# Performance work log

Hardware: AMD Instinct MI355X
Metric: run time of the kernel (lower is better)

Reference implementation:

```python
import jax, jax.numpy as jnp
import numpy as np

B, S, D, H, L = 2, 4096, 768, 12, 4
DFF, WIN, MAXPOS = 3072, 256, 4098
DH = D // H
W1 = WIN // 2            # one-sided window = 128
NC = S // W1             # number of query chunks = 32
EPS = 1e-12              # LongformerConfig default layer_norm_eps
SCALE = 1.0 / float(np.sqrt(DH))


def _ln(x, g, b):
    m = x.mean(-1, keepdims=True)
    v = ((x - m) ** 2).mean(-1, keepdims=True)
    return (x - m) / jnp.sqrt(v + EPS) * g + b


def _fwd(inputs, lengths, pos_emb, tok_emb, ln_emb_g, ln_emb_b,
         Wq, bq, Wk, bk, Wv, bv, Wo, bo, ln1_g, ln1_b,
         Wi, bi, Wf, bf, ln2_g, ln2_b):
    # embeddings: roberta-style position ids start at padding_idx+1 = 2
    x = inputs + pos_emb[2:2 + S][None] + tok_emb[0][None, None]
    x = _ln(x, ln_emb_g, ln_emb_b)

    mask = jnp.arange(S)[None, :] < lengths[:, None]            # [B,S] valid tokens
    idx = jnp.arange(NC)[:, None] * W1 + jnp.arange(3 * W1)     # [NC,3W] into padded keys
    jglob = idx - W1                                            # global key positions
    key_valid = (jglob >= 0)[None] & (jglob[None] < lengths[:, None, None])  # [B,NC,3W]
    qpos = jnp.arange(W1)[:, None]
    kpos = jnp.arange(3 * W1)[None, :]
    band = (kpos >= qpos) & (kpos <= qpos + 2 * W1)             # [W,3W] sliding band
    valid = band[None, None, None] & key_valid[:, None, :, None, :]  # [B,1,NC,W,3W]
    qmask = mask.reshape(B, NC, W1).astype(inputs.dtype)

    for l in range(L):
        q = (x @ Wq[l] + bq[l]).reshape(B, S, H, DH) * SCALE
        k = (x @ Wk[l] + bk[l]).reshape(B, S, H, DH)
        v = (x @ Wv[l] + bv[l]).reshape(B, S, H, DH)
        kp = jnp.pad(k, ((0, 0), (W1, W1), (0, 0), (0, 0)))
        vp = jnp.pad(v, ((0, 0), (W1, W1), (0, 0), (0, 0)))
        kc = jnp.take(kp, idx, axis=1)                          # [B,NC,3W,H,DH]
        vc = jnp.take(vp, idx, axis=1)
        qc = q.reshape(B, NC, W1, H, DH)
        scores = jnp.einsum('bcqhd,bckhd->bhcqk', qc, kc)       # [B,H,NC,W,3W]
        scores = jnp.where(valid, scores, -1e9)
        probs = jax.nn.softmax(scores, axis=-1)
        probs = probs * qmask[:, None, :, :, None]              # zero padded query rows (HF behavior)
        ctx = jnp.einsum('bhcqk,bckhd->bcqhd', probs, vc).reshape(B, S, D)
        x = _ln(x + ctx @ Wo[l] + bo[l], ln1_g[l], ln1_b[l])
        h = jax.nn.gelu(x @ Wi[l] + bi[l], approximate=False)
        x = _ln(x + h @ Wf[l] + bf[l], ln2_g[l], ln2_b[l])
    return x


def setup_inputs() -> dict:
    ks = jax.random.split(jax.random.key(0), 16)
    s = jnp.float32(0.02)
    f = jax.random.normal
    return {
        'inputs': f(ks[0], (B, S, D), jnp.float32),
        'lengths': jax.random.randint(ks[1], (B,), S // 2, S + 1),
        'pos_emb': s * f(ks[2], (MAXPOS, D), jnp.float32),
        'tok_emb': s * f(ks[3], (1, D), jnp.float32),
        'ln_emb_g': jnp.ones((D,), jnp.float32), 'ln_emb_b': jnp.zeros((D,), jnp.float32),
        'Wq': s * f(ks[4], (L, D, D), jnp.float32), 'bq': jnp.zeros((L, D), jnp.float32),
        'Wk': s * f(ks[5], (L, D, D), jnp.float32), 'bk': jnp.zeros((L, D), jnp.float32),
        'Wv': s * f(ks[6], (L, D, D), jnp.float32), 'bv': jnp.zeros((L, D), jnp.float32),
        'Wo': s * f(ks[7], (L, D, D), jnp.float32), 'bo': jnp.zeros((L, D), jnp.float32),
        'ln1_g': jnp.ones((L, D), jnp.float32), 'ln1_b': jnp.zeros((L, D), jnp.float32),
        'Wi': s * f(ks[8], (L, D, DFF), jnp.float32), 'bi': jnp.zeros((L, DFF), jnp.float32),
        'Wf': s * f(ks[9], (L, DFF, D), jnp.float32), 'bf': jnp.zeros((L, D), jnp.float32),
        'ln2_g': jnp.ones((L, D), jnp.float32), 'ln2_b': jnp.zeros((L, D), jnp.float32),
    }


def reference(inputs, lengths, pos_emb, tok_emb, ln_emb_g, ln_emb_b,
              Wq, bq, Wk, bk, Wv, bv, Wo, bo, ln1_g, ln1_b,
              Wi, bi, Wf, bf, ln2_g, ln2_b):
    return _fwd(inputs, lengths, pos_emb, tok_emb, ln_emb_g, ln_emb_b,
                Wq, bq, Wk, bk, Wv, bv, Wo, bo, ln1_g, ln1_b,
                Wi, bi, Wf, bf, ln2_g, ln2_b)
```

## Files before the change

### kernel.cpp

```cpp
#include <hip/hip_runtime.h>
#include <cstdint>

#define S_LEN 4096
#define D_MODEL 768
#define NHEAD 12
#define DHE 64
#define DFF_ 3072
#define NL 4
#define W1_ 128
#define NC_ 32
#define QKVN 2304

typedef __attribute__((ext_vector_type(8))) short v8s;
typedef __attribute__((ext_vector_type(4))) short v4s;
typedef __attribute__((ext_vector_type(4))) float v4f;

__device__ __forceinline__ short f2bf(float f) {
  union { float f; unsigned u; } x; x.f = f;
  unsigned r = x.u + 0x7fffu + ((x.u >> 16) & 1u);
  return (short)(r >> 16);
}

__device__ __forceinline__ float b2f(short s) {
  union { unsigned u; float f; } x; x.u = ((unsigned)(unsigned short)s) << 16;
  return x.f;
}

__device__ __forceinline__ void load_lds16(const short* g, short* l) {
  __builtin_amdgcn_global_load_lds((const __attribute__((address_space(1))) void*)g,
                                   (__attribute__((address_space(3))) void*)l, 16, 0, 0);
}

template<int EPI>
__global__ __launch_bounds__(256, 2)
void gemm128(const short* __restrict__ A, const short* __restrict__ Bt,
             const float* __restrict__ bias, void* __restrict__ outp,
             int M, int N, int K)
{
  __shared__ short sA[2][128 * 64];
  __shared__ short sB[2][128 * 64];
  const int tid = threadIdx.x;
  const int lane = tid & 63, wid = tid >> 6;
  const int g = lane >> 4, l16 = lane & 15;
  const int wr = wid >> 1, wc = wid & 1;
  const int nt = K >> 6;

  const int gx = gridDim.x;
  const int nwg = gx * gridDim.y;
  const int p = blockIdx.y * gx + blockIdx.x;
  const int q8 = nwg >> 3;
  const int lb = (p & 7) * q8 + (p >> 3);
  const int bn_ = lb % gx, bm_ = lb / gx;

  const short* Ab = A + (size_t)(bm_ * 128) * K;
  const short* Bb = Bt + (size_t)(bn_ * 128) * K;

  auto stage = [&](int t, int bufi) {
#pragma unroll
    for (int i = 0; i < 4; ++i) {
      const int byte = i * 4096 + tid * 16;
      const int row = byte >> 7;
      const int lir = (byte & 127) ^ ((row & 7) << 4);
      const int wbase = (i * 4096 + wid * 1024) >> 1;
      load_lds16(Ab + (size_t)row * K + t * 64 + (lir >> 1), &sA[bufi][wbase]);
    }
#pragma unroll
    for (int i = 0; i < 4; ++i) {
      const int byte = i * 4096 + tid * 16;
      const int row = byte >> 7;
      const int lir = (byte & 127) ^ ((row & 7) << 4);
      const int wbase = (i * 4096 + wid * 1024) >> 1;
      load_lds16(Bb + (size_t)row * K + t * 64 + (lir >> 1), &sB[bufi][wbase]);
    }
  };

  auto ldf = [&](const short* plane, int row, int kk) -> v8s {
    const int b = (kk * 64 + g * 16) ^ ((row & 7) << 4);
    return *(const v8s*)((const char*)plane + row * 128 + b);
  };

  v4f acc[4][4] = {};

  stage(0, 0);
  stage(1, 1);
  asm volatile("s_waitcnt vmcnt(8)" ::: "memory");
  __builtin_amdgcn_s_barrier();

  for (int t = 0; t < nt; ++t) {
    const int cur = t & 1;
    const short* pA = sA[cur];
    const short* pB = sB[cur];
    v8s fa[2][4], fb[2][4];
#pragma unroll
    for (int kk = 0; kk < 2; ++kk) {
#pragma unroll
      for (int m = 0; m < 4; ++m) fa[kk][m] = ldf(pA, wr * 64 + m * 16 + l16, kk);
#pragma unroll
      for (int n = 0; n < 4; ++n) fb[kk][n] = ldf(pB, wc * 64 + n * 16 + l16, kk);
    }
    asm volatile("s_waitcnt lgkmcnt(0)" ::: "memory");
    __builtin_amdgcn_sched_barrier(0);
    __builtin_amdgcn_s_barrier();
    if (t + 2 < nt) stage(t + 2, cur);
    __builtin_amdgcn_sched_barrier(0);
    __builtin_amdgcn_s_setprio(1);
#pragma unroll
    for (int kk = 0; kk < 2; ++kk)
#pragma unroll
      for (int m = 0; m < 4; ++m)
#pragma unroll
        for (int n = 0; n < 4; ++n)
          acc[m][n] = __builtin_amdgcn_mfma_f32_16x16x32_bf16(fa[kk][m], fb[kk][n], acc[m][n], 0, 0, 0);
    __builtin_amdgcn_s_setprio(0);
    __builtin_amdgcn_sched_barrier(0);
    if (t + 2 < nt)      asm volatile("s_waitcnt vmcnt(8)" ::: "memory");
    else if (t + 1 < nt) asm volatile("s_waitcnt vmcnt(0)" ::: "memory");
    if (t + 1 < nt) __builtin_amdgcn_s_barrier();
  }

  const int row0 = bm_ * 128 + wr * 64;
  const int col0 = bn_ * 128 + wc * 64;
#pragma unroll
  for (int m = 0; m < 4; ++m)
#pragma unroll
    for (int n = 0; n < 4; ++n) {
      const int col = col0 + n * 16 + l16;
      const float bc = bias[col];
#pragma unroll
      for (int r = 0; r < 4; ++r) {
        const int row = row0 + m * 16 + g * 4 + r;
        const float v = acc[m][n][r] + bc;
        if (EPI == 0) {
          ((short*)outp)[(size_t)row * N + col] = f2bf(v);
        } else {
          const float e = __expf(1.5957691216057308f * (v + 0.044715f * v * v * v));
          ((short*)outp)[(size_t)row * N + col] = f2bf(v - v / (1.0f + e));
        }
      }
    }
}

__global__ __launch_bounds__(256)
void transpose_w(const float* __restrict__ in, short* __restrict__ out, int K, int N,
                 size_t in_ls, size_t out_ls, float scale)
{
  __shared__ float t[32][33];
  const int n0 = blockIdx.x * 32, k0 = blockIdx.y * 32;
  const float* src = in + (size_t)blockIdx.z * in_ls;
  short* dst = out + (size_t)blockIdx.z * out_ls;
  const int tx = threadIdx.x, ty = threadIdx.y;
#pragma unroll
  for (int i = 0; i < 4; ++i)
    t[ty + 8*i][tx] = src[(size_t)(k0 + ty + 8*i) * N + n0 + tx];
  __syncthreads();
#pragma unroll
  for (int i = 0; i < 4; ++i)
    dst[(size_t)(n0 + ty + 8*i) * K + k0 + tx] = f2bf(t[tx][ty + 8*i] * scale);
}

__global__ void prep_bias(const float* __restrict__ bq, const float* __restrict__ bk,
                          const float* __restrict__ bv, float* __restrict__ out)
{
  const int l = blockIdx.x, p = blockIdx.y, c = threadIdx.x;
  const float* s = p == 0 ? bq : (p == 1 ? bk : bv);
  out[(l * 3 + p) * 768 + c] = s[l * 768 + c] * (p == 0 ? 0.125f : 1.0f);
}

__global__ __launch_bounds__(512)
void vtrans(const short* __restrict__ qkv, short* __restrict__ vt)
{
  __shared__ short t[64][65];
  const int s0 = blockIdx.x * 64, h = blockIdx.y, b = blockIdx.z;
  const int tx = threadIdx.x, ty = threadIdx.y;
#pragma unroll
  for (int i = 0; i < 8; ++i)
    t[ty + 8*i][tx] = qkv[(size_t)(b * S_LEN + s0 + ty + 8*i) * QKVN + 1536 + h * DHE + tx];
  __syncthreads();
#pragma unroll
  for (int i = 0; i < 8; ++i)
    vt[((size_t)(b * NHEAD + h) * DHE + ty + 8*i) * S_LEN + s0 + tx] = t[tx][ty + 8*i];
}

template<int MODE>
__global__ __launch_bounds__(256)
void ln_kernel(const float* __restrict__ in0, const void* __restrict__ in1,
               const float* __restrict__ in2,
               const float* __restrict__ gamma, const float* __restrict__ beta,
               float* __restrict__ outf, short* __restrict__ outb)
{
  __shared__ float red[8];
  const int row = blockIdx.x;
  const int tid = threadIdx.x;
  const int wave = tid >> 6, lane = tid & 63;
  float v[3];
#pragma unroll
  for (int i = 0; i < 3; ++i) {
    const int c = tid + i * 256;
    const size_t idx = (size_t)row * D_MODEL + c;
    if (MODE == 0) {
      const int s = row & (S_LEN - 1);
      v[i] = in0[idx] + ((const float*)in1)[(size_t)(2 + s) * D_MODEL + c] + in2[c];
    } else {
      v[i] = in0[idx] + b2f(((const short*)in1)[idx]);
    }
  }
  float sum = v[0] + v[1] + v[2];
#pragma unroll
  for (int m = 1; m < 64; m <<= 1) sum += __shfl_xor(sum, m, 64);
  if (lane == 0) red[wave] = sum;
  __syncthreads();
  const float mean = (red[0] + red[1] + red[2] + red[3]) * (1.0f / 768.0f);
  float sq = 0.f;
#pragma unroll
  for (int i = 0; i < 3; ++i) { float d = v[i] - mean; sq += d * d; }
#pragma unroll
  for (int m = 1; m < 64; m <<= 1) sq += __shfl_xor(sq, m, 64);
  if (lane == 0) red[4 + wave] = sq;
  __syncthreads();
  const float var = (red[4] + red[5] + red[6] + red[7]) * (1.0f / 768.0f);
  const float rstd = 1.0f / sqrtf(var + 1e-12f);
#pragma unroll
  for (int i = 0; i < 3; ++i) {
    const int c = tid + i * 256;
    const size_t idx = (size_t)row * D_MODEL + c;
    const float o = (v[i] - mean) * rstd * gamma[c] + beta[c];
    outf[idx] = o;
    outb[idx] = f2bf(o);
  }
}

__global__ __launch_bounds__(256, 2)
void att_fused(const short* __restrict__ qkv, const short* __restrict__ vt,
               const int* __restrict__ lengths, short* __restrict__ ctx)
{
  __shared__ __align__(16) short KP[320 * 64];
  __shared__ __align__(16) short Vl[64 * 320];
  const int p = blockIdx.x;
  const int lb = (p & 7) * 192 + (p >> 3);
  const int hq = lb & 1, c = (lb >> 1) & 31, bh = lb >> 6;
  const int b = bh / 12, h = bh - b * 12;
  const int len = lengths[b];
  const int tid = threadIdx.x;
  const int wave = tid >> 6, lane = tid & 63;
  const int g = lane >> 4, l16 = lane & 15;
  const int j0h = c * W1_ + hq * 64 - W1_;

  {
    const int row0 = tid >> 3;
    const int o = (tid & 7) * 16;
    const char* kcol = (const char*)qkv + (size_t)b * S_LEN * 4608 + 1536 + h * 128;
#pragma unroll
    for (int i = 0; i < 10; ++i) {
      const int r_ = i * 32 + row0;
      const int op = o ^ ((r_ & 7) << 4);
      int jg = j0h + r_;
      jg = jg < 0 ? 0 : (jg > S_LEN - 1 ? S_LEN - 1 : jg);
      load_lds16((const short*)(kcol + (size_t)jg * 4608 + op),
                 (short*)((char*)KP + i * 4096 + wave * 1024));
    }
  }
  {
    const char* vrow = (const char*)vt + ((size_t)(b * NHEAD + h) * DHE) * (S_LEN * 2);
#pragma unroll
    for (int r = 0; r < 10; ++r) {
      const int off = r * 4096 + tid * 16;
      const int rw = (int)(((unsigned)off * 6554u) >> 22);
      const int o = off - rw * 640;
      int jb = j0h * 2 + (o ^ ((rw & 7) << 4));
      jb = jb < 0 ? 0 : (jb > S_LEN * 2 - 16 ? S_LEN * 2 - 16 : jb);
      load_lds16((const short*)(vrow + (size_t)rw * (S_LEN * 2) + jb),
                 (short*)((char*)Vl + r * 4096 + wave * 1024));
    }
  }
  const int qrow = c * W1_ + hq * 64 + wave * 16 + l16;
  const short* qp = qkv + (size_t)(b * S_LEN + qrow) * QKVN + h * DHE;
  const v8s a0 = *(const v8s*)(qp + g * 8);
  const v8s a1 = *(const v8s*)(qp + 32 + g * 8);

  asm volatile("s_waitcnt vmcnt(0)" ::: "memory");
  __builtin_amdgcn_sched_barrier(0);
  __builtin_amdgcn_s_barrier();

  v4f s[20];
  const int kswz = (l16 & 7) << 4;
#pragma unroll
  for (int nt = 0; nt < 20; ++nt) {
    const char* krow = (const char*)KP + (nt * 16 + l16) * 128;
    const v8s k0 = *(const v8s*)(krow + ((g * 16) ^ kswz));
    const v8s k1 = *(const v8s*)(krow + ((64 + g * 16) ^ kswz));
    v4f t = {0.f, 0.f, 0.f, 0.f};
    t = __builtin_amdgcn_mfma_f32_16x16x32_bf16(k0, a0, t, 0, 0, 0);
    t = __builtin_amdgcn_mfma_f32_16x16x32_bf16(k1, a1, t, 0, 0, 0);
    s[nt] = t;
  }

  const int qloc = wave * 16 + l16;
  float m = -3.0e38f;
#pragma unroll
  for (int nt = 0; nt < 20; ++nt)
#pragma unroll
    for (int r = 0; r < 4; ++r) {
      const int j = nt * 16 + g * 4 + r;
      const int jg = j0h + j;
      const bool ok = (j >= qloc) & (j <= qloc + 2 * W1_) & (jg >= 0) & (jg < len);
      const float v = ok ? s[nt][r] : -1e9f;
      s[nt][r] = v;
      m = fmaxf(m, v);
    }
  m = fmaxf(m, __shfl_xor(m, 16, 64));
  m = fmaxf(m, __shfl_xor(m, 32, 64));
  float su = 0.f;
#pragma unroll
  for (int nt = 0; nt < 20; ++nt)
#pragma unroll
    for (int r = 0; r < 4; ++r) {
      const float e = __expf(s[nt][r] - m);
      s[nt][r] = e;
      su += e;
    }
  su += __shfl_xor(su, 16, 64);
  su += __shfl_xor(su, 32, 64);
  const float f = (qrow < len) ? 1.0f / su : 0.0f;

  __builtin_amdgcn_s_barrier();
  const int pswz = (qloc & 7) << 4;
  char* prow = (char*)KP + qloc * 640;
#pragma unroll
  for (int nt = 0; nt < 20; ++nt) {
    v4s pk;
#pragma unroll
    for (int r = 0; r < 4; ++r) pk[r] = f2bf(s[nt][r] * f);
    *(v4s*)(prow + ((nt * 32 + g * 8) ^ pswz)) = pk;
  }
  asm volatile("s_waitcnt lgkmcnt(0)" ::: "memory");
  __builtin_amdgcn_sched_barrier(0);

  v4f acc[4] = {};
#pragma unroll
  for (int kc = 0; kc < 10; ++kc) {
    const v8s fa = *(const v8s*)(prow + ((kc * 64 + g * 16) ^ pswz));
#pragma unroll
    for (int dt = 0; dt < 4; ++dt) {
      const int vr = dt * 16 + l16;
      const v8s fb = *(const v8s*)((char*)Vl + vr * 640 + ((kc * 64 + g * 16) ^ ((vr & 7) << 4)));
      acc[dt] = __builtin_amdgcn_mfma_f32_16x16x32_bf16(fa, fb, acc[dt], 0, 0, 0);
    }
  }
  const int srow0 = c * W1_ + hq * 64 + wave * 16;
#pragma unroll
  for (int dt = 0; dt < 4; ++dt)
#pragma unroll
    for (int r = 0; r < 4; ++r)
      ctx[(size_t)(b * S_LEN + srow0 + g * 4 + r) * D_MODEL + h * DHE + dt * 16 + l16] = f2bf(acc[dt][r]);
}

extern "C" void kernel_launch(void* const* d_in, const int* in_sizes, int n_in,
                              void* d_out, int out_size, void* d_ws, size_t ws_size,
                              hipStream_t stream) {
  (void)in_sizes; (void)n_in; (void)out_size; (void)ws_size;
  const float* inputs  = (const float*)d_in[0];
  const int*   lengths = (const int*)d_in[1];
  const float* pos_emb = (const float*)d_in[2];
  const float* tok_emb = (const float*)d_in[3];
  const float* ln_emb_g = (const float*)d_in[4];
  const float* ln_emb_b = (const float*)d_in[5];
  const float* Wq = (const float*)d_in[6];
  const float* bq = (const float*)d_in[7];
  const float* Wk = (const float*)d_in[8];
  const float* bk = (const float*)d_in[9];
  const float* Wv = (const float*)d_in[10];
  const float* bv = (const float*)d_in[11];
  const float* Wo = (const float*)d_in[12];
  const float* bo = (const float*)d_in[13];
  const float* ln1_g = (const float*)d_in[14];
  const float* ln1_b = (const float*)d_in[15];
  const float* Wi = (const float*)d_in[16];
  const float* bi = (const float*)d_in[17];
  const float* Wf = (const float*)d_in[18];
  const float* bf2 = (const float*)d_in[19];
  const float* ln2_g = (const float*)d_in[20];
  const float* ln2_b = (const float*)d_in[21];

  const size_t MTOK = (size_t)2 * S_LEN;
  const size_t DD  = (size_t)D_MODEL * D_MODEL;
  const size_t DDF = (size_t)D_MODEL * DFF_;

  char* ws = (char*)d_ws;
  size_t off = 0;
  auto alloc = [&](size_t bytes) { void* p = ws + off; off += (bytes + 255) & ~(size_t)255; return p; };

  short* xb    = (short*)alloc(MTOK * D_MODEL * 2);
  short* qkv   = (short*)alloc(MTOK * QKVN * 2);
  short* vtb   = (short*)alloc(MTOK * D_MODEL * 2);
  short* yb    = (short*)alloc(MTOK * D_MODEL * 2);
  short* ctxb  = (short*)alloc(MTOK * D_MODEL * 2);
  short* hb    = (short*)alloc(MTOK * DFF_ * 2);
  short* wqkvt = (short*)alloc((size_t)NL * QKVN * D_MODEL * 2);
  short* wot   = (short*)alloc((size_t)NL * DD * 2);
  short* wit   = (short*)alloc((size_t)NL * DDF * 2);
  short* wft   = (short*)alloc((size_t)NL * DDF * 2);
  float* bqkv  = (float*)alloc((size_t)NL * QKVN * 4);
  float* x = (float*)d_out;

  const dim3 tb(32, 8);
  const size_t QL = (size_t)QKVN * D_MODEL;
  transpose_w<<<dim3(24, 24, NL), tb, 0, stream>>>(Wq, wqkvt,            D_MODEL, D_MODEL, DD, QL, 0.125f);
  transpose_w<<<dim3(24, 24, NL), tb, 0, stream>>>(Wk, wqkvt + 768*768,  D_MODEL, D_MODEL, DD, QL, 1.0f);
  transpose_w<<<dim3(24, 24, NL), tb, 0, stream>>>(Wv, wqkvt + 1536*768, D_MODEL, D_MODEL, DD, QL, 1.0f);
  transpose_w<<<dim3(24, 24, NL), tb, 0, stream>>>(Wo, wot, D_MODEL, D_MODEL, DD, DD, 1.0f);
  transpose_w<<<dim3(96, 24, NL), tb, 0, stream>>>(Wi, wit, D_MODEL, DFF_, DDF, DDF, 1.0f);
  transpose_w<<<dim3(24, 96, NL), tb, 0, stream>>>(Wf, wft, DFF_, D_MODEL, DDF, DDF, 1.0f);
  prep_bias<<<dim3(NL, 3), 768, 0, stream>>>(bq, bk, bv, bqkv);

  ln_kernel<0><<<MTOK, 256, 0, stream>>>(inputs, pos_emb, tok_emb, ln_emb_g, ln_emb_b, x, xb);

  for (int l = 0; l < NL; ++l) {
    gemm128<0><<<dim3(18, 64), 256, 0, stream>>>(xb, wqkvt + (size_t)l * QL, bqkv + (size_t)l * QKVN,
                                                 qkv, (int)MTOK, QKVN, D_MODEL);
    vtrans<<<dim3(64, NHEAD, 2), dim3(64, 8), 0, stream>>>(qkv, vtb);
    att_fused<<<dim3(1536), 256, 0, stream>>>(qkv, vtb, lengths, ctxb);
    gemm128<0><<<dim3(6, 64), 256, 0, stream>>>(ctxb, wot + (size_t)l * DD, bo + l * D_MODEL,
                                                yb, (int)MTOK, D_MODEL, D_MODEL);
    ln_kernel<1><<<MTOK, 256, 0, stream>>>(x, yb, nullptr, ln1_g + l * D_MODEL, ln1_b + l * D_MODEL, x, xb);
    gemm128<2><<<dim3(24, 64), 256, 0, stream>>>(xb, wit + (size_t)l * DDF, bi + l * DFF_,
                                                 hb, (int)MTOK, DFF_, D_MODEL);
    gemm128<0><<<dim3(6, 64), 256, 0, stream>>>(hb, wft + (size_t)l * DDF, bf2 + l * D_MODEL,
                                                yb, (int)MTOK, D_MODEL, DFF_);
    ln_kernel<1><<<MTOK, 256, 0, stream>>>(x, yb, nullptr, ln2_g + l * D_MODEL, ln2_b + l * D_MODEL, x, xb);
  }
}
```

Before: 895.5 us.

## Use 128x64 GEMM tiles for N=768 projections and reorder the MFMA/stage pipeline

Templates the GEMM on N tile width so the two N=768 GEMMs (output projection and FFN down) use 128x64 tiles. That doubles their grid from 384 to 768 workgroups, which fills the CUs better, and raises the occupancy hint to 3. The main loop is also reordered: MFMAs now issue right after the LDS fragment reads, without an explicit lgkmcnt wait, and the next stage's global-to-LDS loads are issued after the barrier that follows the compute. This trades more A-tile reloads and less overlap of the prefetch with the MFMAs for better load balance.

```diff
diff --git a/kernel.cpp b/kernel.cpp
--- a/kernel.cpp
+++ b/kernel.cpp
@@ -31,14 +31,17 @@
                                    (__attribute__((address_space(3))) void*)l, 16, 0, 0);
 }
 
-template<int EPI>
-__global__ __launch_bounds__(256, 2)
+template<int NB, int EPI>
+__global__ __launch_bounds__(256, NB == 64 ? 3 : 2)
 void gemm128(const short* __restrict__ A, const short* __restrict__ Bt,
              const float* __restrict__ bias, void* __restrict__ outp,
              int M, int N, int K)
 {
+  constexpr int NF = NB / 32;
+  constexpr int BI = NB / 32;
+  constexpr int SI = 4 + BI;
   __shared__ short sA[2][128 * 64];
-  __shared__ short sB[2][128 * 64];
+  __shared__ short sB[2][NB * 64];
   const int tid = threadIdx.x;
   const int lane = tid & 63, wid = tid >> 6;
   const int g = lane >> 4, l16 = lane & 15;
@@ -53,7 +56,7 @@
   const int bn_ = lb % gx, bm_ = lb / gx;
 
   const short* Ab = A + (size_t)(bm_ * 128) * K;
-  const short* Bb = Bt + (size_t)(bn_ * 128) * K;
+  const short* Bb = Bt + (size_t)(bn_ * NB) * K;
 
   auto stage = [&](int t, int bufi) {
 #pragma unroll
@@ -65,7 +68,7 @@
       load_lds16(Ab + (size_t)row * K + t * 64 + (lir >> 1), &sA[bufi][wbase]);
     }
 #pragma unroll
-    for (int i = 0; i < 4; ++i) {
+    for (int i = 0; i < BI; ++i) {
       const int byte = i * 4096 + tid * 16;
       const int row = byte >> 7;
       const int lir = (byte & 127) ^ ((row & 7) << 4);
@@ -79,51 +82,58 @@
     return *(const v8s*)((const char*)plane + row * 128 + b);
   };
 
-  v4f acc[4][4] = {};
+  v4f acc[4][NF] = {};
 
   stage(0, 0);
   stage(1, 1);
-  asm volatile("s_waitcnt vmcnt(8)" ::: "memory");
+  if constexpr (NB == 128) asm volatile("s_waitcnt vmcnt(8)" ::: "memory");
+  else                     asm volatile("s_waitcnt vmcnt(6)" ::: "memory");
   __builtin_amdgcn_s_barrier();
+  __builtin_amdgcn_sched_barrier(0);
 
   for (int t = 0; t < nt; ++t) {
     const int cur = t & 1;
     const short* pA = sA[cur];
     const short* pB = sB[cur];
-    v8s fa[2][4], fb[2][4];
+    v8s fa[2][4], fb[2][NF];
 #pragma unroll
     for (int kk = 0; kk < 2; ++kk) {
 #pragma unroll
       for (int m = 0; m < 4; ++m) fa[kk][m] = ldf(pA, wr * 64 + m * 16 + l16, kk);
 #pragma unroll
-      for (int n = 0; n < 4; ++n) fb[kk][n] = ldf(pB, wc * 64 + n * 16 + l16, kk);
-    }
-    asm volatile("s_waitcnt lgkmcnt(0)" ::: "memory");
+      for (int n = 0; n < NF; ++n) fb[kk][n] = ldf(pB, wc * (NF * 16) + n * 16 + l16, kk);
+    }
+    __builtin_amdgcn_s_setprio(1);
+#pragma unroll
+    for (int kk = 0; kk < 2; ++kk)
+#pragma unroll
+      for (int m = 0; m < 4; ++m)
+#pragma unroll
+        for (int n = 0; n < NF; ++n)
+          acc[m][n] = __builtin_amdgcn_mfma_f32_16x16x32_bf16(fa[kk][m], fb[kk][n], acc[m][n], 0, 0, 0);
+    __builtin_amdgcn_s_setprio(0);
+    __builtin_amdgcn_s_barrier();
     __builtin_amdgcn_sched_barrier(0);
-    __builtin_amdgcn_s_barrier();
     if (t + 2 < nt) stage(t + 2, cur);
     __builtin_amdgcn_sched_barrier(0);
-    __builtin_amdgcn_s_setprio(1);
-#pragma unroll
-    for (int kk = 0; kk < 2; ++kk)
-#pragma unroll
-      for (int m = 0; m < 4; ++m)
-#pragma unroll
-        for (int n = 0; n < 4; ++n)
-          acc[m][n] = __builtin_amdgcn_mfma_f32_16x16x32_bf16(fa[kk][m], fb[kk][n], acc[m][n], 0, 0, 0);
-    __builtin_amdgcn_s_setprio(0);
-    __builtin_amdgcn_sched_barrier(0);
-    if (t + 2 < nt)      asm volatile("s_waitcnt vmcnt(8)" ::: "memory");
-    else if (t + 1 < nt) asm volatile("s_waitcnt vmcnt(0)" ::: "memory");
-    if (t + 1 < nt) __builtin_amdgcn_s_barrier();
+    if (t + 2 < nt) {
+      if constexpr (NB == 128) asm volatile("s_waitcnt vmcnt(8)" ::: "memory");
+      else                     asm volatile("s_waitcnt vmcnt(6)" ::: "memory");
+    } else if (t + 1 < nt) {
+      asm volatile("s_waitcnt vmcnt(0)" ::: "memory");
+    }
+    if (t + 1 < nt) {
+      __builtin_amdgcn_s_barrier();
+      __builtin_amdgcn_sched_barrier(0);
+    }
   }
 
   const int row0 = bm_ * 128 + wr * 64;
-  const int col0 = bn_ * 128 + wc * 64;
+  const int col0 = bn_ * NB + wc * (NF * 16);
 #pragma unroll
   for (int m = 0; m < 4; ++m)
 #pragma unroll
-    for (int n = 0; n < 4; ++n) {
+    for (int n = 0; n < NF; ++n) {
       const int col = col0 + n * 16 + l16;
       const float bc = bias[col];
 #pragma unroll
@@ -415,17 +425,17 @@
   ln_kernel<0><<<MTOK, 256, 0, stream>>>(inputs, pos_emb, tok_emb, ln_emb_g, ln_emb_b, x, xb);
 
   for (int l = 0; l < NL; ++l) {
-    gemm128<0><<<dim3(18, 64), 256, 0, stream>>>(xb, wqkvt + (size_t)l * QL, bqkv + (size_t)l * QKVN,
-                                                 qkv, (int)MTOK, QKVN, D_MODEL);
+    gemm128<128, 0><<<dim3(18, 64), 256, 0, stream>>>(xb, wqkvt + (size_t)l * QL, bqkv + (size_t)l * QKVN,
+                                                      qkv, (int)MTOK, QKVN, D_MODEL);
     vtrans<<<dim3(64, NHEAD, 2), dim3(64, 8), 0, stream>>>(qkv, vtb);
     att_fused<<<dim3(1536), 256, 0, stream>>>(qkv, vtb, lengths, ctxb);
-    gemm128<0><<<dim3(6, 64), 256, 0, stream>>>(ctxb, wot + (size_t)l * DD, bo + l * D_MODEL,
-                                                yb, (int)MTOK, D_MODEL, D_MODEL);
+    gemm128<64, 0><<<dim3(12, 64), 256, 0, stream>>>(ctxb, wot + (size_t)l * DD, bo + l * D_MODEL,
+                                                     yb, (int)MTOK, D_MODEL, D_MODEL);
     ln_kernel<1><<<MTOK, 256, 0, stream>>>(x, yb, nullptr, ln1_g + l * D_MODEL, ln1_b + l * D_MODEL, x, xb);
-    gemm128<2><<<dim3(24, 64), 256, 0, stream>>>(xb, wit + (size_t)l * DDF, bi + l * DFF_,
-                                                 hb, (int)MTOK, DFF_, D_MODEL);
-    gemm128<0><<<dim3(6, 64), 256, 0, stream>>>(hb, wft + (size_t)l * DDF, bf2 + l * D_MODEL,
-                                                yb, (int)MTOK, D_MODEL, DFF_);
+    gemm128<128, 2><<<dim3(24, 64), 256, 0, stream>>>(xb, wit + (size_t)l * DDF, bi + l * DFF_,
+                                                      hb, (int)MTOK, DFF_, D_MODEL);
+    gemm128<64, 0><<<dim3(12, 64), 256, 0, stream>>>(hb, wft + (size_t)l * DDF, bf2 + l * D_MODEL,
+                                                     yb, (int)MTOK, D_MODEL, DFF_);
     ln_kernel<1><<<MTOK, 256, 0, stream>>>(x, yb, nullptr, ln2_g + l * D_MODEL, ln2_b + l * D_MODEL, x, xb);
   }
 }
```

New measurement: 949.2 us. 6.0% more time.
